# Optimization experiments

Measured on AMD Instinct MI355X. Metric: run time of the kernel, lower is better.

The kernel has to match this reference:

```python
import jax, jax.numpy as jnp
import numpy as np

DIM = 192
D_STATE = 16
D_CONV = 4
EXPAND = 2
D_INNER = DIM * EXPAND          # 384
DT_RANK = (DIM + 15) // 16      # 12
B_SZ, H_SP, W_SP = 4, 64, 64


def setup_inputs() -> dict:
    key = jax.random.key(0)
    ks = jax.random.split(key, 8)
    f = jax.random.normal
    return {
        "x": f(ks[0], (B_SZ, DIM, H_SP, W_SP), jnp.float32),
        "ln_w": jnp.ones((DIM,), jnp.float32),
        "ln_b": jnp.zeros((DIM,), jnp.float32),
        "in_proj_w": f(ks[1], (2 * D_INNER, DIM), jnp.float32) * 0.02,
        "conv_w": f(ks[2], (D_INNER, D_CONV), jnp.float32) * 0.2,
        "conv_b": jnp.zeros((D_INNER,), jnp.float32),
        "x_proj_w": f(ks[3], (DT_RANK + 2 * D_STATE, D_INNER), jnp.float32) * 0.02,
        "dt_proj_w": f(ks[4], (D_INNER, DT_RANK), jnp.float32) * 0.1,
        "dt_proj_b": f(ks[5], (D_INNER,), jnp.float32) * 0.1,
        "A_log": jnp.log(jnp.broadcast_to(
            jnp.arange(1, D_STATE + 1, dtype=jnp.float32), (D_INNER, D_STATE))),
        "D": jnp.ones((D_INNER,), jnp.float32),
        "out_proj_w": f(ks[6], (DIM, D_INNER), jnp.float32) * 0.02,
    }


def _mamba_block(x, ln_w, ln_b, in_proj_w, conv_w, conv_b, x_proj_w,
                 dt_proj_w, dt_proj_b, A_log, D, out_proj_w):
    B, C, H, W = x.shape
    L = H * W
    # [B,C,H,W] -> [B,L,C]
    xf = x.transpose(0, 2, 3, 1).reshape(B, L, C)

    # LayerNorm
    mu = xf.mean(-1, keepdims=True)
    var = ((xf - mu) ** 2).mean(-1, keepdims=True)
    xn = (xf - mu) * jax.lax.rsqrt(var + 1e-5) * ln_w + ln_b

    # in_proj -> xm (ssm branch), z (gate branch)
    xz = xn @ in_proj_w.T                      # [B,L,2*Di]
    xm, z = jnp.split(xz, 2, axis=-1)

    # causal depthwise conv1d over sequence (pad left d_conv-1)
    xc = xm.transpose(0, 2, 1)                 # [B,Di,L]
    xc = jax.lax.conv_general_dilated(
        xc, conv_w[:, None, :], (1,), [(D_CONV - 1, 0)],
        dimension_numbers=("NCH", "OIH", "NCH"),
        feature_group_count=D_INNER)
    xc = xc + conv_b[None, :, None]
    xm = jax.nn.silu(xc.transpose(0, 2, 1))    # [B,L,Di]

    # x_proj -> dt, B, C (input-dependent SSM params)
    dbc = xm @ x_proj_w.T                      # [B,L,dt_rank+2N]
    dt, Bm, Cm = jnp.split(dbc, [DT_RANK, DT_RANK + D_STATE], axis=-1)
    dt = jax.nn.softplus(dt @ dt_proj_w.T + dt_proj_b)  # [B,L,Di]

    A = -jnp.exp(A_log)                        # [Di,N]

    def step(h, inp):
        xt, dtt, Bt, Ct = inp                  # [B,Di],[B,Di],[B,N],[B,N]
        dA = jnp.exp(dtt[..., None] * A)       # [B,Di,N]
        h = h * dA + (dtt * xt)[..., None] * Bt[:, None, :]
        y = jnp.einsum('bdn,bn->bd', h, Ct)
        return h, y

    h0 = jnp.zeros((B, D_INNER, D_STATE), xm.dtype)
    scan_in = (xm.transpose(1, 0, 2), dt.transpose(1, 0, 2),
               Bm.transpose(1, 0, 2), Cm.transpose(1, 0, 2))
    _, ys = jax.lax.scan(step, h0, scan_in)    # [L,B,Di]

    y = ys.transpose(1, 0, 2) + xm * D         # skip term D*x
    y = y * jax.nn.silu(z)                     # gate
    out = y @ out_proj_w.T                     # [B,L,C]

    out = xf + out                             # residual
    return out.reshape(B, H, W, C).transpose(0, 3, 1, 2)


def reference(x, ln_w, ln_b, in_proj_w, conv_w, conv_b, x_proj_w,
              dt_proj_w, dt_proj_b, A_log, D, out_proj_w):
    return _mamba_block(x, ln_w, ln_b, in_proj_w, conv_w, conv_b, x_proj_w,
                        dt_proj_w, dt_proj_b, A_log, D, out_proj_w)
```

## Files before the change

kernel.cpp:

```cpp
#include <hip/hip_runtime.h>
#include <hip/hip_bf16.h>
#include <cstdint>
#include <cmath>

#define DIMC   192
#define DSTATE 16
#define DCONV  4
#define DINNER 384
#define DTRANK 12
#define BSZ    4
#define HSP    64
#define WSP    64
#define LSEQ   4096
#define NTOK   (BSZ*LSEQ)
#define XZW    (2*DINNER)
#define LC5    32
#define NCH5   (LSEQ/LC5)
#define NXP    448

typedef unsigned short ushortT;
using short8 = __attribute__((ext_vector_type(8))) short;
using f32x4  = __attribute__((ext_vector_type(4))) float;

typedef unsigned int u32_as1 __attribute__((address_space(1)));
typedef unsigned int u32_as3 __attribute__((address_space(3)));

__device__ __forceinline__ void gl_lds16(const ushortT* g, ushortT* l) {
  __builtin_amdgcn_global_load_lds((const u32_as1*)g, (u32_as3*)l, 16, 0, 0);
}

__device__ __forceinline__ float bflo(unsigned u) { return __uint_as_float(u << 16); }
__device__ __forceinline__ float bfhi(unsigned u) { return __uint_as_float(u & 0xffff0000u); }
__device__ __forceinline__ float bf2f(ushortT u) { return __uint_as_float(((unsigned)u) << 16); }
__device__ __forceinline__ unsigned pkbf(float lo, float hi) {
  __hip_bfloat16 l = __float2bfloat16(lo), h = __float2bfloat16(hi);
  return (unsigned)*(ushortT*)&l | ((unsigned)*(ushortT*)&h << 16);
}
#define UNPK8(arr, base, v4)                                        \
  arr[base + 0] = bflo(v4.x); arr[base + 1] = bfhi(v4.x);           \
  arr[base + 2] = bflo(v4.y); arr[base + 3] = bfhi(v4.y);           \
  arr[base + 4] = bflo(v4.z); arr[base + 5] = bfhi(v4.z);           \
  arr[base + 6] = bflo(v4.w); arr[base + 7] = bfhi(v4.w);

__global__ __launch_bounds__(512) void ln_prep_kernel(
    const float* __restrict__ x, const float* __restrict__ ln_w,
    const float* __restrict__ ln_b, const float* __restrict__ w_in,
    const float* __restrict__ w_out, const float* __restrict__ xpw,
    const float* __restrict__ dtw, __hip_bfloat16* __restrict__ xn,
    __hip_bfloat16* __restrict__ wbf, __hip_bfloat16* __restrict__ wcb) {
  if (blockIdx.x >= 256) {
    int gid = (blockIdx.x - 256) * 512 + threadIdx.x;
    if (gid < 221184) {
      float v = gid < 147456 ? w_in[gid] : w_out[gid - 147456];
      wbf[gid] = __float2bfloat16(v);
    } else {
      int e = gid - 221184;
      int dd = e / 384, k = e % 384;
      float v = 0.f;
      if (dd < 384) {
#pragma unroll
        for (int j = 0; j < 12; ++j) v = fmaf(dtw[dd * 12 + j], xpw[j * 384 + k], v);
      } else if (dd < 416) {
        v = xpw[(dd - 372) * 384 + k];
      }
      wcb[e] = __float2bfloat16(v);
    }
    return;
  }
  __shared__ float xs[DIMC][WSP + 1];
  __shared__ float mu_s[WSP], rs_s[WSP];
  int bh = blockIdx.x;
  int b = bh >> 6, h = bh & 63;
  int tid = threadIdx.x;
  const float* xb = x + (size_t)b * DIMC * LSEQ + (size_t)h * WSP;
  for (int e = tid; e < DIMC * WSP; e += 512) {
    int c = e >> 6, w = e & 63;
    xs[c][w] = xb[(size_t)c * LSEQ + w];
  }
  __syncthreads();
  {
    int w = tid >> 3, p = tid & 7;
    float s = 0.f, s2 = 0.f;
#pragma unroll
    for (int i = 0; i < 24; ++i) {
      float v = xs[p * 24 + i][w];
      s += v; s2 = fmaf(v, v, s2);
    }
    s  += __shfl_xor(s, 1);  s2 += __shfl_xor(s2, 1);
    s  += __shfl_xor(s, 2);  s2 += __shfl_xor(s2, 2);
    s  += __shfl_xor(s, 4);  s2 += __shfl_xor(s2, 4);
    if (p == 0) {
      float mu = s * (1.f / DIMC);
      float var = s2 * (1.f / DIMC) - mu * mu;
      mu_s[w] = mu;
      rs_s[w] = rsqrtf(var + 1e-5f);
    }
  }
  __syncthreads();
  __hip_bfloat16* xo = xn + (size_t)(b * LSEQ + h * WSP) * DIMC;
  for (int e = tid; e < DIMC * WSP; e += 512) {
    int w = e / DIMC, c = e % DIMC;
    xo[(size_t)w * DIMC + c] =
        __float2bfloat16((xs[c][w] - mu_s[w]) * rs_s[w] * ln_w[c] + ln_b[c]);
  }
}

template<int WM, int WN, int FM, int FN, int EPI>
__global__ __launch_bounds__(256) void gemm_bf16(
    const ushortT* __restrict__ A, const ushortT* __restrict__ B,
    void* __restrict__ Cv, void* __restrict__ Cv2,
    const ushortT* __restrict__ xm_aux, const float* __restrict__ bias384,
    const float* __restrict__ xres, int K, int Nreal, int ldc) {
  constexpr int BM = WM * FM * 16, BN = WN * FN * 16;
  __shared__ ushortT As[BM][64];
  __shared__ ushortT Bs[BN][64];
  __shared__ float Ct[(EPI == 1) ? (BM * (BN + 4)) : 1];
  int bm = blockIdx.x * BM, bn = blockIdx.y * BN;
  int tid = threadIdx.x, lane = tid & 63, w = tid >> 6;
  int wm = w / WN, wn = w % WN;
  int lm = lane & 15, lk = lane >> 4;
  int sub = lane >> 3, slot = lane & 7;
  const ushortT* Bb = B;
  size_t zoff = 0;
  if constexpr (EPI == 1) {
    size_t zb = blockIdx.z;
    Bb = B + zb * (size_t)LSEQ * K;
    zoff = zb * (size_t)DIMC * LSEQ;
  }
  f32x4 acc[FM][FN];
#pragma unroll
  for (int mi = 0; mi < FM; ++mi)
#pragma unroll
    for (int ni = 0; ni < FN; ++ni) acc[mi][ni] = (f32x4){0.f, 0.f, 0.f, 0.f};

  for (int k0 = 0; k0 < K; k0 += 64) {
    __syncthreads();
#pragma unroll
    for (int j = 0; j < BM / 32; ++j) {
      int row = w * (BM / 4) + j * 8;
      gl_lds16(A + (size_t)(bm + row + sub) * K + k0 + ((slot ^ sub) << 3),
               &As[row][0]);
    }
#pragma unroll
    for (int j = 0; j < BN / 32; ++j) {
      int row = w * (BN / 4) + j * 8;
      gl_lds16(Bb + (size_t)(bn + row + sub) * K + k0 + ((slot ^ sub) << 3),
               &Bs[row][0]);
    }
    __syncthreads();
#pragma unroll
    for (int ks = 0; ks < 2; ++ks) {
      short8 af[FM], bfr[FN];
#pragma unroll
      for (int mi = 0; mi < FM; ++mi) {
        int row = wm * FM * 16 + mi * 16 + lm;
        int col = (ks * 64 + lk * 16) ^ ((lm & 7) << 4);
        af[mi] = *(const short8*)((const char*)As + row * 128 + col);
      }
#pragma unroll
      for (int ni = 0; ni < FN; ++ni) {
        int row = wn * FN * 16 + ni * 16 + lm;
        int col = (ks * 64 + lk * 16) ^ ((lm & 7) << 4);
        bfr[ni] = *(const short8*)((const char*)Bs + row * 128 + col);
      }
#pragma unroll
      for (int mi = 0; mi < FM; ++mi)
#pragma unroll
        for (int ni = 0; ni < FN; ++ni)
          acc[mi][ni] = __builtin_amdgcn_mfma_f32_16x16x32_bf16(
              af[mi], bfr[ni], acc[mi][ni], 0, 0, 0);
    }
  }

  if constexpr (EPI == 1) {
    __syncthreads();
    float (*CtA)[BN + 4] = (float(*)[BN + 4])Ct;
#pragma unroll
    for (int mi = 0; mi < FM; ++mi)
#pragma unroll
      for (int ni = 0; ni < FN; ++ni)
#pragma unroll
        for (int r = 0; r < 4; ++r)
          CtA[wm * FM * 16 + mi * 16 + lk * 4 + r][wn * FN * 16 + ni * 16 + lm] =
              acc[mi][ni][r];
    __syncthreads();
    float* Cout = (float*)Cv;
    for (int e = tid; e < BM * (BN / 4); e += 256) {
      int row = e / (BN / 4), q = e % (BN / 4);
      size_t gidx = zoff + (size_t)(bm + row) * LSEQ + bn + q * 4;
      float4 rv = *(const float4*)(xres + gidx);
      float4 o;
      o.x = CtA[row][q * 4 + 0] + rv.x;
      o.y = CtA[row][q * 4 + 1] + rv.y;
      o.z = CtA[row][q * 4 + 2] + rv.z;
      o.w = CtA[row][q * 4 + 3] + rv.w;
      *(float4*)(Cout + gidx) = o;
    }
  } else {
#pragma unroll
    for (int mi = 0; mi < FM; ++mi) {
#pragma unroll
      for (int ni = 0; ni < FN; ++ni) {
        int ncol = bn + wn * FN * 16 + ni * 16 + lm;
#pragma unroll
        for (int r = 0; r < 4; ++r) {
          int m = bm + wm * FM * 16 + mi * 16 + lk * 4 + r;
          if constexpr (EPI == 2) {
            if (ncol < Nreal)
              ((__hip_bfloat16*)Cv)[(size_t)m * ldc + ncol] =
                  __float2bfloat16(acc[mi][ni][r]);
          } else {
            if (ncol < 384) {
              float dtr = acc[mi][ni][r] + bias384[ncol];
              float dt = dtr > 15.f ? dtr : __logf(1.f + __expf(dtr));
              float xmv = bf2f(xm_aux[(size_t)m * DINNER + ncol]);
              ((unsigned*)Cv)[(size_t)m * DINNER + ncol] = pkbf(dt, xmv);
            } else if (ncol < 416) {
              __hip_bfloat16 bv = __float2bfloat16(acc[mi][ni][r]);
              ((ushortT*)Cv2)[(size_t)m * 48 + 16 + (ncol - 384)] = *(ushortT*)&bv;
            }
          }
        }
      }
    }
  }
}

__global__ __launch_bounds__(256) void conv_silu_kernel(
    const __hip_bfloat16* __restrict__ xz, const float* __restrict__ conv_w,
    const float* __restrict__ conv_b, __hip_bfloat16* __restrict__ xmh) {
  int g8 = blockIdx.x * 256 + threadIdx.x;
  int d8 = g8 % 48;
  int tok = g8 / 48;
  int l = tok & (LSEQ - 1);
  int d0 = d8 * 8;
  const ushortT* base = (const ushortT*)xz + (size_t)tok * XZW + d0;
  uint4 r0, r1, r2, r3;
  r3 = *(const uint4*)(base);
  r2 = l >= 1 ? *(const uint4*)(base - XZW)     : (uint4){0, 0, 0, 0};
  r1 = l >= 2 ? *(const uint4*)(base - 2 * XZW) : (uint4){0, 0, 0, 0};
  r0 = l >= 3 ? *(const uint4*)(base - 3 * XZW) : (uint4){0, 0, 0, 0};
  float x0[8], x1[8], x2[8], x3[8];
  UNPK8(x0, 0, r0) UNPK8(x1, 0, r1) UNPK8(x2, 0, r2) UNPK8(x3, 0, r3)
  ushortT outv[8];
#pragma unroll
  for (int j = 0; j < 8; ++j) {
    const float4 w = *(const float4*)(conv_w + (d0 + j) * 4);
    float acc = conv_b[d0 + j];
    acc = fmaf(w.x, x0[j], acc);
    acc = fmaf(w.y, x1[j], acc);
    acc = fmaf(w.z, x2[j], acc);
    acc = fmaf(w.w, x3[j], acc);
    float s = acc / (1.f + __expf(-acc));
    __hip_bfloat16 sb = __float2bfloat16(s);
    outv[j] = *(ushortT*)&sb;
  }
  *(uint4*)((ushortT*)xmh + (size_t)tok * DINNER + d0) = *(uint4*)outv;
}

__global__ __launch_bounds__(384) void scan_part1(
    const unsigned* __restrict__ dxpk, const ushortT* __restrict__ dbc,
    const float* __restrict__ A_log, unsigned* __restrict__ hpk) {
  __shared__ ushortT dbc_s[32 * 48];
  int d = threadIdx.x, c = blockIdx.x, b = blockIdx.y;
  size_t rowbase = (size_t)b * LSEQ + (size_t)c * LC5;
  if (d < 192) {
    int row = d / 6, q = d % 6;
    ((uint4*)dbc_s)[d] = ((const uint4*)(dbc + (rowbase + row) * 48))[q];
  }
  float Ac2[16];
#pragma unroll
  for (int q = 0; q < 4; ++q) {
    float4 t4 = *(const float4*)(A_log + d * 16 + q * 4);
    Ac2[q * 4 + 0] = -__expf(t4.x) * 1.44269504f;
    Ac2[q * 4 + 1] = -__expf(t4.y) * 1.44269504f;
    Ac2[q * 4 + 2] = -__expf(t4.z) * 1.44269504f;
    Ac2[q * 4 + 3] = -__expf(t4.w) * 1.44269504f;
  }
  float h[16];
#pragma unroll
  for (int n = 0; n < 16; ++n) h[n] = 0.f;
  float sdt = 0.f;
  const unsigned* pkp = dxpk + rowbase * DINNER + d;
  __syncthreads();
#pragma unroll
  for (int t0 = 0; t0 < LC5; t0 += 4) {
    unsigned pk[4];
#pragma unroll
    for (int j = 0; j < 4; ++j) pk[j] = pkp[(t0 + j) * DINNER];
#pragma unroll
    for (int j = 0; j < 4; ++j) {
      int t = t0 + j;
      float dtt = bflo(pk[j]), xmv = bfhi(pk[j]);
      sdt += dtt;
      float dx = dtt * xmv;
      const char* bb = (const char*)dbc_s + t * 96;
      uint4 B0 = *(const uint4*)(bb + 32);
      uint4 B1 = *(const uint4*)(bb + 48);
      float Bv[16];
      UNPK8(Bv, 0, B0)
      UNPK8(Bv, 8, B1)
#pragma unroll
      for (int n = 0; n < 16; ++n) {
        float a = __builtin_amdgcn_exp2f(dtt * Ac2[n]);
        h[n] = fmaf(h[n], a, dx * Bv[n]);
      }
    }
  }
  unsigned up[16];
#pragma unroll
  for (int n = 0; n < 16; ++n)
    up[n] = pkbf(h[n], __builtin_amdgcn_exp2f(Ac2[n] * sdt));
  uint4* hp4 = (uint4*)(hpk + (((size_t)b * NCH5 + c) * DINNER + d) * 16);
#pragma unroll
  for (int q = 0; q < 4; ++q) hp4[q] = *(uint4*)&up[q * 4];
}

__global__ __launch_bounds__(256) void scan_part2(
    const unsigned* __restrict__ hpk, ushortT* __restrict__ hinb) {
  int e = blockIdx.x * 256 + threadIdx.x;
  int b = blockIdx.y;
  float H = 0.f;
  size_t base = (size_t)b * NCH5 * (DINNER * DSTATE) + e;
#pragma unroll 16
  for (int c = 0; c < NCH5; ++c) {
    size_t idx = base + (size_t)c * (DINNER * DSTATE);
    unsigned w = hpk[idx];
    __hip_bfloat16 hb = __float2bfloat16(H);
    hinb[idx] = *(ushortT*)&hb;
    H = fmaf(bfhi(w), H, bflo(w));
  }
}

__global__ __launch_bounds__(384) void scan_part3(
    const unsigned* __restrict__ dxpk, const ushortT* __restrict__ dbc,
    const __hip_bfloat16* __restrict__ xz, const float* __restrict__ A_log,
    const float* __restrict__ Dvec, const ushortT* __restrict__ hinb,
    __hip_bfloat16* __restrict__ ybuf) {
  __shared__ ushortT dbc_s[32 * 48];
  int d = threadIdx.x, c = blockIdx.x, b = blockIdx.y;
  size_t rowbase = (size_t)b * LSEQ + (size_t)c * LC5;
  if (d < 192) {
    int row = d / 6, q = d % 6;
    ((uint4*)dbc_s)[d] = ((const uint4*)(dbc + (rowbase + row) * 48))[q];
  }
  float Ac2[16];
#pragma unroll
  for (int q = 0; q < 4; ++q) {
    float4 t4 = *(const float4*)(A_log + d * 16 + q * 4);
    Ac2[q * 4 + 0] = -__expf(t4.x) * 1.44269504f;
    Ac2[q * 4 + 1] = -__expf(t4.y) * 1.44269504f;
    Ac2[q * 4 + 2] = -__expf(t4.z) * 1.44269504f;
    Ac2[q * 4 + 3] = -__expf(t4.w) * 1.44269504f;
  }
  float h[16];
  {
    const uint4* hp = (const uint4*)(hinb + (((size_t)b * NCH5 + c) * DINNER + d) * 16);
    uint4 h0 = hp[0], h1 = hp[1];
    UNPK8(h, 0, h0)
    UNPK8(h, 8, h1)
  }
  float Dd = Dvec[d];
  const unsigned* pkp = dxpk + rowbase * DINNER + d;
  const ushortT* zp = (const ushortT*)xz + rowbase * XZW + DINNER + d;
  __hip_bfloat16* yp = ybuf + rowbase * DINNER + d;
  __syncthreads();
#pragma unroll
  for (int t0 = 0; t0 < LC5; t0 += 4) {
    unsigned pk[4];
    ushortT zv4[4];
#pragma unroll
    for (int j = 0; j < 4; ++j) {
      pk[j] = pkp[(t0 + j) * DINNER];
      zv4[j] = zp[(t0 + j) * XZW];
    }
#pragma unroll
    for (int j = 0; j < 4; ++j) {
      int t = t0 + j;
      float dtt = bflo(pk[j]), xmv = bfhi(pk[j]);
      float dx = dtt * xmv;
      const char* bb = (const char*)dbc_s + t * 96;
      uint4 B0 = *(const uint4*)(bb + 32);
      uint4 B1 = *(const uint4*)(bb + 48);
      uint4 C0 = *(const uint4*)(bb + 64);
      uint4 C1 = *(const uint4*)(bb + 80);
      float Bv[16], Cw[16];
      UNPK8(Bv, 0, B0)
      UNPK8(Bv, 8, B1)
      UNPK8(Cw, 0, C0)
      UNPK8(Cw, 8, C1)
      float y0 = 0.f, y1 = 0.f, y2 = 0.f, y3 = 0.f;
#pragma unroll
      for (int n = 0; n < 16; n += 4) {
        float a0 = __builtin_amdgcn_exp2f(dtt * Ac2[n + 0]);
        float a1 = __builtin_amdgcn_exp2f(dtt * Ac2[n + 1]);
        float a2 = __builtin_amdgcn_exp2f(dtt * Ac2[n + 2]);
        float a3 = __builtin_amdgcn_exp2f(dtt * Ac2[n + 3]);
        h[n + 0] = fmaf(h[n + 0], a0, dx * Bv[n + 0]);
        h[n + 1] = fmaf(h[n + 1], a1, dx * Bv[n + 1]);
        h[n + 2] = fmaf(h[n + 2], a2, dx * Bv[n + 2]);
        h[n + 3] = fmaf(h[n + 3], a3, dx * Bv[n + 3]);
        y0 = fmaf(h[n + 0], Cw[n + 0], y0);
        y1 = fmaf(h[n + 1], Cw[n + 1], y1);
        y2 = fmaf(h[n + 2], Cw[n + 2], y2);
        y3 = fmaf(h[n + 3], Cw[n + 3], y3);
      }
      float yv = fmaf(xmv, Dd, (y0 + y1) + (y2 + y3));
      float zv = bf2f(zv4[j]);
      float gt = zv * __builtin_amdgcn_rcpf(
          1.f + __builtin_amdgcn_exp2f(zv * -1.44269504f));
      yp[(size_t)t * DINNER] = __float2bfloat16(yv * gt);
    }
  }
}

extern "C" void kernel_launch(void* const* d_in, const int* in_sizes, int n_in,
                              void* d_out, int out_size, void* d_ws, size_t ws_size,
                              hipStream_t stream) {
  const float* x        = (const float*)d_in[0];
  const float* ln_w     = (const float*)d_in[1];
  const float* ln_b     = (const float*)d_in[2];
  const float* in_proj  = (const float*)d_in[3];
  const float* conv_w   = (const float*)d_in[4];
  const float* conv_b   = (const float*)d_in[5];
  const float* x_proj   = (const float*)d_in[6];
  const float* dt_w     = (const float*)d_in[7];
  const float* dt_b     = (const float*)d_in[8];
  const float* A_log    = (const float*)d_in[9];
  const float* Dvec     = (const float*)d_in[10];
  const float* out_proj = (const float*)d_in[11];
  float* out = (float*)d_out;

  float* ws = (float*)d_ws;
  __hip_bfloat16* xzb  = (__hip_bfloat16*)ws;
  __hip_bfloat16* xmh  = (__hip_bfloat16*)(ws + 6291456);
  ushortT*        dbcb = (ushortT*)(ws + 9437184);
  unsigned*       dxpk = (unsigned*)(ws + 9830400);
  unsigned*       hpk  = (unsigned*)(ws + 16121856);
  ushortT*        hinb = (ushortT*)(ws + 19267584);
  __hip_bfloat16* ybuf = (__hip_bfloat16*)(ws + 20840448);
  __hip_bfloat16* xnbf = (__hip_bfloat16*)(ws + 23986176);
  __hip_bfloat16* wbf  = (__hip_bfloat16*)(ws + 25559040);
  __hip_bfloat16* wcb  = (__hip_bfloat16*)(ws + 25669632);

  const ushortT* win  = (const ushortT*)wbf;
  const ushortT* wout = (const ushortT*)(wbf + 147456);

  ln_prep_kernel<<<1024, 512, 0, stream>>>(
      x, ln_w, ln_b, in_proj, out_proj, x_proj, dt_w, xnbf, wbf, wcb);

  gemm_bf16<2, 2, 4, 4, 2><<<dim3(NTOK / 128, XZW / 128), 256, 0, stream>>>(
      (const ushortT*)xnbf, win, xzb, nullptr, nullptr, nullptr, nullptr,
      DIMC, XZW, XZW);

  conv_silu_kernel<<<(NTOK * DINNER / 8) / 256, 256, 0, stream>>>(
      xzb, conv_w, conv_b, xmh);

  gemm_bf16<2, 2, 4, 2, 4><<<dim3(NTOK / 128, NXP / 64), 256, 0, stream>>>(
      (const ushortT*)xmh, (const ushortT*)wcb, dxpk, dbcb,
      (const ushortT*)xmh, dt_b, nullptr, DINNER, NXP, 0);

  scan_part1<<<dim3(NCH5, BSZ), 384, 0, stream>>>(dxpk, dbcb, A_log, hpk);
  scan_part2<<<dim3(DINNER * DSTATE / 256, BSZ), 256, 0, stream>>>(hpk, hinb);
  scan_part3<<<dim3(NCH5, BSZ), 384, 0, stream>>>(
      dxpk, dbcb, xzb, A_log, Dvec, hinb, ybuf);

  gemm_bf16<2, 2, 2, 4, 1><<<dim3(DIMC / 64, LSEQ / 128, BSZ), 256, 0, stream>>>(
      wout, (const ushortT*)ybuf, out, nullptr, nullptr, nullptr, x,
      DINNER, LSEQ, LSEQ);
}
```

Baseline: 141.9 us.

## Compute dt projection inside scan kernels instead of via folded GEMM output

The x_proj GEMM no longer multiplies by the folded dt_proj weight, which produced a 448-wide output including a packed dt/xm buffer. It now outputs only the 44 low-rank columns (dt_rank, B, C) into the 48-wide dbc buffer. Both scan kernels recompute dt from the 12 low-rank values with a per-channel dot product plus softplus, and read xm directly. This cuts GEMM FLOPs and a large intermediate write/read, at the cost of extra ALU work and softplus evaluated twice in the scan passes.

```diff
diff --git a/kernel.cpp b/kernel.cpp
--- a/kernel.cpp
+++ b/kernel.cpp
@@ -16,7 +16,6 @@
 #define XZW    (2*DINNER)
 #define LC5    32
 #define NCH5   (LSEQ/LC5)
-#define NXP    448
 
 typedef unsigned short ushortT;
 using short8 = __attribute__((ext_vector_type(8))) short;
@@ -46,24 +45,18 @@
     const float* __restrict__ x, const float* __restrict__ ln_w,
     const float* __restrict__ ln_b, const float* __restrict__ w_in,
     const float* __restrict__ w_out, const float* __restrict__ xpw,
-    const float* __restrict__ dtw, __hip_bfloat16* __restrict__ xn,
-    __hip_bfloat16* __restrict__ wbf, __hip_bfloat16* __restrict__ wcb) {
+    __hip_bfloat16* __restrict__ xn,
+    __hip_bfloat16* __restrict__ wbf, __hip_bfloat16* __restrict__ wxp) {
   if (blockIdx.x >= 256) {
     int gid = (blockIdx.x - 256) * 512 + threadIdx.x;
     if (gid < 221184) {
       float v = gid < 147456 ? w_in[gid] : w_out[gid - 147456];
       wbf[gid] = __float2bfloat16(v);
-    } else {
+    } else if (gid < 221184 + 24576) {
       int e = gid - 221184;
       int dd = e / 384, k = e % 384;
-      float v = 0.f;
-      if (dd < 384) {
-#pragma unroll
-        for (int j = 0; j < 12; ++j) v = fmaf(dtw[dd * 12 + j], xpw[j * 384 + k], v);
-      } else if (dd < 416) {
-        v = xpw[(dd - 372) * 384 + k];
-      }
-      wcb[e] = __float2bfloat16(v);
+      float v = dd < 44 ? xpw[dd * 384 + k] : 0.f;
+      wxp[e] = __float2bfloat16(v);
     }
     return;
   }
@@ -108,9 +101,8 @@
 template<int WM, int WN, int FM, int FN, int EPI>
 __global__ __launch_bounds__(256) void gemm_bf16(
     const ushortT* __restrict__ A, const ushortT* __restrict__ B,
-    void* __restrict__ Cv, void* __restrict__ Cv2,
-    const ushortT* __restrict__ xm_aux, const float* __restrict__ bias384,
-    const float* __restrict__ xres, int K, int Nreal, int ldc) {
+    void* __restrict__ Cv, const float* __restrict__ xres,
+    int K, int Nreal, int ldc) {
   constexpr int BM = WM * FM * 16, BN = WN * FN * 16;
   __shared__ ushortT As[BM][64];
   __shared__ ushortT Bs[BN][64];
@@ -210,14 +202,10 @@
               ((__hip_bfloat16*)Cv)[(size_t)m * ldc + ncol] =
                   __float2bfloat16(acc[mi][ni][r]);
           } else {
-            if (ncol < 384) {
-              float dtr = acc[mi][ni][r] + bias384[ncol];
-              float dt = dtr > 15.f ? dtr : __logf(1.f + __expf(dtr));
-              float xmv = bf2f(xm_aux[(size_t)m * DINNER + ncol]);
-              ((unsigned*)Cv)[(size_t)m * DINNER + ncol] = pkbf(dt, xmv);
-            } else if (ncol < 416) {
-              __hip_bfloat16 bv = __float2bfloat16(acc[mi][ni][r]);
-              ((ushortT*)Cv2)[(size_t)m * 48 + 16 + (ncol - 384)] = *(ushortT*)&bv;
+            if (ncol < 44) {
+              int nc2 = ncol < 12 ? ncol : ncol + 4;
+              ((__hip_bfloat16*)Cv)[(size_t)m * 48 + nc2] =
+                  __float2bfloat16(acc[mi][ni][r]);
             }
           }
         }
@@ -259,7 +247,8 @@
 }
 
 __global__ __launch_bounds__(384) void scan_part1(
-    const unsigned* __restrict__ dxpk, const ushortT* __restrict__ dbc,
+    const __hip_bfloat16* __restrict__ xmh, const ushortT* __restrict__ dbc,
+    const float* __restrict__ dtw, const float* __restrict__ dtb,
     const float* __restrict__ A_log, unsigned* __restrict__ hpk) {
   __shared__ ushortT dbc_s[32 * 48];
   int d = threadIdx.x, c = blockIdx.x, b = blockIdx.y;
@@ -268,6 +257,11 @@
     int row = d / 6, q = d % 6;
     ((uint4*)dbc_s)[d] = ((const uint4*)(dbc + (rowbase + row) * 48))[q];
   }
+  float w12[12];
+  *(float4*)&w12[0] = *(const float4*)(dtw + d * 12);
+  *(float4*)&w12[4] = *(const float4*)(dtw + d * 12 + 4);
+  *(float4*)&w12[8] = *(const float4*)(dtw + d * 12 + 8);
+  float bias = dtb[d];
   float Ac2[16];
 #pragma unroll
   for (int q = 0; q < 4; ++q) {
@@ -281,20 +275,28 @@
 #pragma unroll
   for (int n = 0; n < 16; ++n) h[n] = 0.f;
   float sdt = 0.f;
-  const unsigned* pkp = dxpk + rowbase * DINNER + d;
+  const ushortT* xp = (const ushortT*)xmh + rowbase * DINNER + d;
   __syncthreads();
 #pragma unroll
   for (int t0 = 0; t0 < LC5; t0 += 4) {
-    unsigned pk[4];
-#pragma unroll
-    for (int j = 0; j < 4; ++j) pk[j] = pkp[(t0 + j) * DINNER];
+    ushortT xm4[4];
+#pragma unroll
+    for (int j = 0; j < 4; ++j) xm4[j] = xp[(t0 + j) * DINNER];
 #pragma unroll
     for (int j = 0; j < 4; ++j) {
       int t = t0 + j;
-      float dtt = bflo(pk[j]), xmv = bfhi(pk[j]);
+      const char* bb = (const char*)dbc_s + t * 96;
+      uint4 D0 = *(const uint4*)(bb);
+      uint4 D1 = *(const uint4*)(bb + 16);
+      float dv[16];
+      UNPK8(dv, 0, D0)
+      UNPK8(dv, 8, D1)
+      float v = bias;
+#pragma unroll
+      for (int jj = 0; jj < 12; ++jj) v = fmaf(dv[jj], w12[jj], v);
+      float dtt = v > 15.f ? v : __logf(1.f + __expf(v));
       sdt += dtt;
-      float dx = dtt * xmv;
-      const char* bb = (const char*)dbc_s + t * 96;
+      float dx = dtt * bf2f(xm4[j]);
       uint4 B0 = *(const uint4*)(bb + 32);
       uint4 B1 = *(const uint4*)(bb + 48);
       float Bv[16];
@@ -333,8 +335,9 @@
 }
 
 __global__ __launch_bounds__(384) void scan_part3(
-    const unsigned* __restrict__ dxpk, const ushortT* __restrict__ dbc,
-    const __hip_bfloat16* __restrict__ xz, const float* __restrict__ A_log,
+    const __hip_bfloat16* __restrict__ xmh, const ushortT* __restrict__ dbc,
+    const __hip_bfloat16* __restrict__ xz, const float* __restrict__ dtw,
+    const float* __restrict__ dtb, const float* __restrict__ A_log,
     const float* __restrict__ Dvec, const ushortT* __restrict__ hinb,
     __hip_bfloat16* __restrict__ ybuf) {
   __shared__ ushortT dbc_s[32 * 48];
@@ -344,6 +347,11 @@
     int row = d / 6, q = d % 6;
     ((uint4*)dbc_s)[d] = ((const uint4*)(dbc + (rowbase + row) * 48))[q];
   }
+  float w12[12];
+  *(float4*)&w12[0] = *(const float4*)(dtw + d * 12);
+  *(float4*)&w12[4] = *(const float4*)(dtw + d * 12 + 4);
+  *(float4*)&w12[8] = *(const float4*)(dtw + d * 12 + 8);
+  float bias = dtb[d];
   float Ac2[16];
 #pragma unroll
   for (int q = 0; q < 4; ++q) {
@@ -361,25 +369,33 @@
     UNPK8(h, 8, h1)
   }
   float Dd = Dvec[d];
-  const unsigned* pkp = dxpk + rowbase * DINNER + d;
+  const ushortT* xp = (const ushortT*)xmh + rowbase * DINNER + d;
   const ushortT* zp = (const ushortT*)xz + rowbase * XZW + DINNER + d;
   __hip_bfloat16* yp = ybuf + rowbase * DINNER + d;
   __syncthreads();
 #pragma unroll
   for (int t0 = 0; t0 < LC5; t0 += 4) {
-    unsigned pk[4];
-    ushortT zv4[4];
+    ushortT xm4[4], zv4[4];
 #pragma unroll
     for (int j = 0; j < 4; ++j) {
-      pk[j] = pkp[(t0 + j) * DINNER];
+      xm4[j] = xp[(t0 + j) * DINNER];
       zv4[j] = zp[(t0 + j) * XZW];
     }
 #pragma unroll
     for (int j = 0; j < 4; ++j) {
       int t = t0 + j;
-      float dtt = bflo(pk[j]), xmv = bfhi(pk[j]);
+      const char* bb = (const char*)dbc_s + t * 96;
+      uint4 D0 = *(const uint4*)(bb);
+      uint4 D1 = *(const uint4*)(bb + 16);
+      float dv[16];
+      UNPK8(dv, 0, D0)
+      UNPK8(dv, 8, D1)
+      float v = bias;
+#pragma unroll
+      for (int jj = 0; jj < 12; ++jj) v = fmaf(dv[jj], w12[jj], v);
+      float dtt = v > 15.f ? v : __logf(1.f + __expf(v));
+      float xmv = bf2f(xm4[j]);
       float dx = dtt * xmv;
-      const char* bb = (const char*)dbc_s + t * 96;
       uint4 B0 = *(const uint4*)(bb + 32);
       uint4 B1 = *(const uint4*)(bb + 48);
       uint4 C0 = *(const uint4*)(bb + 64);
@@ -435,37 +451,35 @@
   __hip_bfloat16* xzb  = (__hip_bfloat16*)ws;
   __hip_bfloat16* xmh  = (__hip_bfloat16*)(ws + 6291456);
   ushortT*        dbcb = (ushortT*)(ws + 9437184);
-  unsigned*       dxpk = (unsigned*)(ws + 9830400);
   unsigned*       hpk  = (unsigned*)(ws + 16121856);
   ushortT*        hinb = (ushortT*)(ws + 19267584);
   __hip_bfloat16* ybuf = (__hip_bfloat16*)(ws + 20840448);
   __hip_bfloat16* xnbf = (__hip_bfloat16*)(ws + 23986176);
   __hip_bfloat16* wbf  = (__hip_bfloat16*)(ws + 25559040);
-  __hip_bfloat16* wcb  = (__hip_bfloat16*)(ws + 25669632);
+  __hip_bfloat16* wxp  = (__hip_bfloat16*)(ws + 25669632);
 
   const ushortT* win  = (const ushortT*)wbf;
   const ushortT* wout = (const ushortT*)(wbf + 147456);
 
-  ln_prep_kernel<<<1024, 512, 0, stream>>>(
-      x, ln_w, ln_b, in_proj, out_proj, x_proj, dt_w, xnbf, wbf, wcb);
+  ln_prep_kernel<<<736, 512, 0, stream>>>(
+      x, ln_w, ln_b, in_proj, out_proj, x_proj, xnbf, wbf, wxp);
 
   gemm_bf16<2, 2, 4, 4, 2><<<dim3(NTOK / 128, XZW / 128), 256, 0, stream>>>(
-      (const ushortT*)xnbf, win, xzb, nullptr, nullptr, nullptr, nullptr,
-      DIMC, XZW, XZW);
+      (const ushortT*)xnbf, win, xzb, nullptr, DIMC, XZW, XZW);
 
   conv_silu_kernel<<<(NTOK * DINNER / 8) / 256, 256, 0, stream>>>(
       xzb, conv_w, conv_b, xmh);
 
-  gemm_bf16<2, 2, 4, 2, 4><<<dim3(NTOK / 128, NXP / 64), 256, 0, stream>>>(
-      (const ushortT*)xmh, (const ushortT*)wcb, dxpk, dbcb,
-      (const ushortT*)xmh, dt_b, nullptr, DINNER, NXP, 0);
-
-  scan_part1<<<dim3(NCH5, BSZ), 384, 0, stream>>>(dxpk, dbcb, A_log, hpk);
+  gemm_bf16<4, 1, 1, 4, 3><<<dim3(NTOK / 64, 1), 256, 0, stream>>>(
+      (const ushortT*)xmh, (const ushortT*)wxp, dbcb, nullptr,
+      DINNER, 44, 48);
+
+  scan_part1<<<dim3(NCH5, BSZ), 384, 0, stream>>>(
+      xmh, dbcb, dt_w, dt_b, A_log, hpk);
   scan_part2<<<dim3(DINNER * DSTATE / 256, BSZ), 256, 0, stream>>>(hpk, hinb);
   scan_part3<<<dim3(NCH5, BSZ), 384, 0, stream>>>(
-      dxpk, dbcb, xzb, A_log, Dvec, hinb, ybuf);
+      xmh, dbcb, xzb, dt_w, dt_b, A_log, Dvec, hinb, ybuf);
 
   gemm_bf16<2, 2, 2, 4, 1><<<dim3(DIMC / 64, LSEQ / 128, BSZ), 256, 0, stream>>>(
-      wout, (const ushortT*)ybuf, out, nullptr, nullptr, nullptr, x,
-      DINNER, LSEQ, LSEQ);
-}
+      wout, (const ushortT*)ybuf, out, x, DINNER, LSEQ, LSEQ);
+}
```

Result: slower. 160.7 us (+13.3%).
